# Kernel optimization log

Hardware: AMD Instinct MI355X
Metric: run time of the kernel (lower is better)

Reference implementation:

```python
import jax, jax.numpy as jnp
from jax import lax
import numpy as np

B, H, Wd, CIN, COUT, KH, KW = 64, 64, 64, 128, 256, 3, 3
WSTD, BSTD = 0.3, 0.3
DN = ('NHWC', 'HWIO', 'NHWC')


def setup_inputs() -> dict:
    key = jax.random.key(0)
    k1, k2, k3, k4, k5 = jax.random.split(key, 5)
    X = jax.random.normal(k1, (B, H, Wd, CIN), dtype=jnp.float32)
    W = jax.random.normal(k2, (KH, KW, CIN, COUT), dtype=jnp.float32) * 0.05
    bias = jax.random.normal(k3, (COUT,), dtype=jnp.float32) * 0.05
    # per-sample multiplicative noise: |1 + N(0, std)| as in the original layer
    Werr = jnp.abs(1.0 + WSTD * jax.random.normal(k4, (B, KH, KW, CIN, COUT), dtype=jnp.float32))
    Berr = jnp.abs(1.0 + BSTD * jax.random.normal(k5, (B, COUT), dtype=jnp.float32))
    return {"X": X, "W": W, "bias": bias, "Werr": Werr, "Berr": Berr}


def _conv_single(x, w):
    # x: [H, W, Cin], w: [kh, kw, Cin, Cout] -> [Ho, Wo, Cout], VALID, stride 1
    return lax.conv_general_dilated(x[None], w, window_strides=(1, 1),
                                    padding='VALID', dimension_numbers=DN)[0]


def reference(X, W, bias, Werr, Berr):
    # per-sample noisy filters: memW[b] = W * Werr[b]
    memW = W[None] * Werr                        # [B, kh, kw, Cin, Cout]
    Z = jax.vmap(_conv_single)(X, memW)          # [B, Ho, Wo, Cout]
    membias = bias[None] * Berr                  # [B, Cout]
    return Z + membias[:, None, None, :]
```

## Files before the change

### kernel.cpp

```cpp
#include <hip/hip_runtime.h>
#include <hip/hip_bf16.h>

#define NB   64
#define NH   64
#define NW   64
#define NCI  128
#define NCO  256
#define NHO  62
#define NWO  62
#define MTOT (NHO*NWO)
#define KTOT (9*NCI)

#define BM  128
#define BN  128
#define BK  32

using bf16x8 = __attribute__((ext_vector_type(8))) short;
using f32x4  = __attribute__((ext_vector_type(4))) float;

__device__ __forceinline__ void gload_lds16(const __hip_bfloat16* g,
                                            __hip_bfloat16* l) {
    __builtin_amdgcn_global_load_lds(
        (const __attribute__((address_space(1))) unsigned int*)g,
        (__attribute__((address_space(3))) unsigned int*)l,
        16, 0, 0);
}

__global__ __launch_bounds__(256)
void cvt_x_kernel(const float* __restrict__ X,
                  __hip_bfloat16* __restrict__ Xb, int n8) {
    int i = blockIdx.x * 256 + threadIdx.x;
    if (i >= n8) return;
    const float4* p = (const float4*)X + (size_t)i * 2;
    float4 a = p[0], c = p[1];
    union { __hip_bfloat16 h[8]; float4 v; } u;
    u.h[0] = __float2bfloat16(a.x); u.h[1] = __float2bfloat16(a.y);
    u.h[2] = __float2bfloat16(a.z); u.h[3] = __float2bfloat16(a.w);
    u.h[4] = __float2bfloat16(c.x); u.h[5] = __float2bfloat16(c.y);
    u.h[6] = __float2bfloat16(c.z); u.h[7] = __float2bfloat16(c.w);
    *((float4*)Xb + i) = u.v;
}

#define TK 64
#define TN 64
#define TPAD 65
__global__ __launch_bounds__(256)
void build_wt_kernel(const float* __restrict__ W,
                     const float* __restrict__ Werr,
                     __hip_bfloat16* __restrict__ Wt) {
    __shared__ __hip_bfloat16 tile[TK * TPAD];
    const int t  = threadIdx.x;
    const int b  = blockIdx.z;
    const int k0 = blockIdx.x * TK;
    const int n0 = blockIdx.y * TN;

    const int c4 = (t & 15) * 4;
    const int r  = t >> 4;
    const float* wb = W + n0;
    const float* eb = Werr + (size_t)b * (KTOT * NCO) + n0;
#pragma unroll
    for (int p = 0; p < 4; p++) {
        int k  = k0 + r + p * 16;
        int kl = r + p * 16;
        float4 w = *(const float4*)(wb + (size_t)k * NCO + c4);
        float4 e = *(const float4*)(eb + (size_t)k * NCO + c4);
        tile[kl * TPAD + c4 + 0] = __float2bfloat16(w.x * e.x);
        tile[kl * TPAD + c4 + 1] = __float2bfloat16(w.y * e.y);
        tile[kl * TPAD + c4 + 2] = __float2bfloat16(w.z * e.z);
        tile[kl * TPAD + c4 + 3] = __float2bfloat16(w.w * e.w);
    }
    __syncthreads();
    const int np = t >> 2;
    const int ks = (t & 3) * 16;
    __hip_bfloat16* ob = Wt + ((size_t)b * NCO + n0 + np) * KTOT + k0 + ks;
    union { __hip_bfloat16 h[8]; float4 v; } u;
#pragma unroll
    for (int h2 = 0; h2 < 2; h2++) {
#pragma unroll
        for (int q = 0; q < 8; q++) u.h[q] = tile[(ks + h2 * 8 + q) * TPAD + np];
        *(float4*)(ob + h2 * 8) = u.v;
    }
}

__global__ __launch_bounds__(256)
void gemm_bf16_kernel(const __hip_bfloat16* __restrict__ Xb,
                      const __hip_bfloat16* __restrict__ Wt,
                      const float* __restrict__ bias,
                      const float* __restrict__ Berr,
                      float* __restrict__ out) {
    __shared__ __hip_bfloat16 As[BM * BK];
    __shared__ __hip_bfloat16 Bs[BN * BK];

    const int t    = threadIdx.x;
    const int lane = t & 63;
    const int wave = t >> 6;
    const int b  = blockIdx.y;
    const int nt = blockIdx.x & 1;
    const int mt = blockIdx.x >> 1;
    const int m0 = mt * BM;
    const int n0 = nt * BN;

    const int seg = (lane & 3) * 8;
    const int rl  = lane >> 2;
    const int rA0 = wave * 32 + rl;
    const int rA1 = rA0 + 16;

    int mA0 = m0 + rA0; if (mA0 > MTOT - 1) mA0 = MTOT - 1;
    int mA1 = m0 + rA1; if (mA1 > MTOT - 1) mA1 = MTOT - 1;
    const int oh0 = mA0 / NWO, ow0 = mA0 % NWO;
    const int oh1 = mA1 / NWO, ow1 = mA1 % NWO;
    const __hip_bfloat16* xbase = Xb + (size_t)b * (NH * NW * NCI);
    const __hip_bfloat16* ga0 = xbase + (oh0 * NW + ow0) * NCI + seg;
    const __hip_bfloat16* ga1 = xbase + (oh1 * NW + ow1) * NCI + seg;
    const __hip_bfloat16* wbase = Wt + ((size_t)b * NCO + n0) * KTOT;
    const __hip_bfloat16* gb0 = wbase + rA0 * KTOT + seg;
    const __hip_bfloat16* gb1 = wbase + rA1 * KTOT + seg;

    __hip_bfloat16* lA0 = As + wave * (32 * BK);
    __hip_bfloat16* lA1 = lA0 + 16 * BK;
    __hip_bfloat16* lB0 = Bs + wave * (32 * BK);
    __hip_bfloat16* lB1 = lB0 + 16 * BK;

    const int wm = wave & 1, wn = wave >> 1;
    const int lrow = lane & 15, quad = lane >> 4;
    const int aoff = (wm * 64 + lrow) * BK + quad * 8;
    const int boff = (wn * 64 + lrow) * BK + quad * 8;

    f32x4 acc[4][4];
#pragma unroll
    for (int i = 0; i < 4; i++)
#pragma unroll
        for (int j = 0; j < 4; j++) acc[i][j] = (f32x4){0.f, 0.f, 0.f, 0.f};

    for (int kk = 0; kk < KTOT; kk += BK) {
        const int kh  = kk / (3 * NCI);
        const int kwp = (kk / NCI) % 3;
        const int ci0 = kk % NCI;
        const int ku  = (kh * NW + kwp) * NCI + ci0;

        gload_lds16(ga0 + ku, lA0);
        gload_lds16(ga1 + ku, lA1);
        gload_lds16(gb0 + kk, lB0);
        gload_lds16(gb1 + kk, lB1);
        __syncthreads();

        bf16x8 af[4], bfr[4];
#pragma unroll
        for (int i = 0; i < 4; i++) af[i]  = *(const bf16x8*)&As[aoff + i * 16 * BK];
#pragma unroll
        for (int j = 0; j < 4; j++) bfr[j] = *(const bf16x8*)&Bs[boff + j * 16 * BK];
#pragma unroll
        for (int i = 0; i < 4; i++)
#pragma unroll
            for (int j = 0; j < 4; j++)
                acc[i][j] = __builtin_amdgcn_mfma_f32_16x16x32_bf16(
                    af[i], bfr[j], acc[i][j], 0, 0, 0);
        __syncthreads();
    }

    float bv[4];
#pragma unroll
    for (int j = 0; j < 4; j++) {
        int n = n0 + wn * 64 + j * 16 + lrow;
        bv[j] = bias[n] * Berr[b * NCO + n];
    }
#pragma unroll
    for (int i = 0; i < 4; i++) {
#pragma unroll
        for (int r = 0; r < 4; r++) {
            int m = m0 + wm * 64 + i * 16 + quad * 4 + r;
            if (m < MTOT) {
                float* op = out + ((size_t)b * MTOT + m) * NCO;
#pragma unroll
                for (int j = 0; j < 4; j++) {
                    int n = n0 + wn * 64 + j * 16 + lrow;
                    op[n] = acc[i][j][r] + bv[j];
                }
            }
        }
    }
}

__global__ void naive_conv_kernel(const float* __restrict__ X,
                                  const float* __restrict__ W,
                                  const float* __restrict__ bias,
                                  const float* __restrict__ Werr,
                                  const float* __restrict__ Berr,
                                  float* __restrict__ out) {
    size_t idx = (size_t)blockIdx.x * 256 + threadIdx.x;
    if (idx >= (size_t)NB * MTOT * NCO) return;
    int n = idx % NCO;
    size_t m = idx / NCO;
    int ow = m % NWO; size_t t2 = m / NWO;
    int oh = t2 % NHO; int b = t2 / NHO;
    float acc = bias[n] * Berr[b * NCO + n];
    for (int kh = 0; kh < 3; kh++)
        for (int kw = 0; kw < 3; kw++) {
            const float* xp = X + (((size_t)b * NH + oh + kh) * NW + ow + kw) * NCI;
            const float* wp = W + ((kh * 3 + kw) * NCI) * (size_t)NCO + n;
            const float* ep = Werr + (size_t)b * KTOT * NCO + ((kh * 3 + kw) * NCI) * (size_t)NCO + n;
            for (int ci = 0; ci < NCI; ci++)
                acc += xp[ci] * wp[ci * NCO] * ep[ci * NCO];
        }
    out[idx] = acc;
}

extern "C" void kernel_launch(void* const* d_in, const int* in_sizes, int n_in,
                              void* d_out, int out_size, void* d_ws, size_t ws_size,
                              hipStream_t stream) {
    const float* X    = (const float*)d_in[0];
    const float* W    = (const float*)d_in[1];
    const float* bias = (const float*)d_in[2];
    const float* Werr = (const float*)d_in[3];
    const float* Berr = (const float*)d_in[4];
    float* out = (float*)d_out;

    const size_t xb_bytes = (size_t)NB * NH * NW * NCI * 2;
    const size_t wt_bytes = (size_t)NB * NCO * KTOT * 2;

    if (ws_size < xb_bytes + wt_bytes) {
        size_t total = (size_t)NB * MTOT * NCO;
        naive_conv_kernel<<<(int)((total + 255) / 256), 256, 0, stream>>>(
            X, W, bias, Werr, Berr, out);
        return;
    }

    __hip_bfloat16* Xb = (__hip_bfloat16*)d_ws;
    __hip_bfloat16* Wt = (__hip_bfloat16*)((char*)d_ws + xb_bytes);

    int n8 = NB * NH * NW * NCI / 8;
    cvt_x_kernel<<<n8 / 256, 256, 0, stream>>>(X, Xb, n8);
    build_wt_kernel<<<dim3(KTOT / TK, NCO / TN, NB), 256, 0, stream>>>(W, Werr, Wt);
    gemm_bf16_kernel<<<dim3(2 * ((MTOT + BM - 1) / BM), NB), 256, 0, stream>>>(
        Xb, Wt, bias, Berr, out);
}
```

Before: 590.0 us.

## Rewrite GEMM with 256x256x64 tiles, LDS double buffering, XOR swizzle and block swizzle

```diff
diff --git a/kernel.cpp b/kernel.cpp
--- a/kernel.cpp
+++ b/kernel.cpp
@@ -11,9 +11,11 @@
 #define MTOT (NHO*NWO)
 #define KTOT (9*NCI)
 
-#define BM  128
-#define BN  128
-#define BK  32
+#define BM  256
+#define BN  256
+#define BK  64
+#define NKT (KTOT/BK)
+#define MT  16
 
 using bf16x8 = __attribute__((ext_vector_type(8))) short;
 using f32x4  = __attribute__((ext_vector_type(4))) float;
@@ -25,6 +27,10 @@
         (__attribute__((address_space(3))) unsigned int*)l,
         16, 0, 0);
 }
+
+#define SBAR()   __builtin_amdgcn_s_barrier()
+#define SCHED()  __builtin_amdgcn_sched_barrier(0)
+#define VMCNT(n) asm volatile("s_waitcnt vmcnt(" #n ")" ::: "memory")
 
 __global__ __launch_bounds__(256)
 void cvt_x_kernel(const float* __restrict__ X,
@@ -82,100 +88,125 @@
     }
 }
 
-__global__ __launch_bounds__(256)
+__global__ __launch_bounds__(512, 2)
 void gemm_bf16_kernel(const __hip_bfloat16* __restrict__ Xb,
                       const __hip_bfloat16* __restrict__ Wt,
                       const float* __restrict__ bias,
                       const float* __restrict__ Berr,
                       float* __restrict__ out) {
-    __shared__ __hip_bfloat16 As[BM * BK];
-    __shared__ __hip_bfloat16 Bs[BN * BK];
+    __shared__ __hip_bfloat16 lds[2][2][BM * BK];
 
     const int t    = threadIdx.x;
     const int lane = t & 63;
     const int wave = t >> 6;
-    const int b  = blockIdx.y;
-    const int nt = blockIdx.x & 1;
-    const int mt = blockIdx.x >> 1;
-    const int m0 = mt * BM;
-    const int n0 = nt * BN;
-
-    const int seg = (lane & 3) * 8;
-    const int rl  = lane >> 2;
-    const int rA0 = wave * 32 + rl;
-    const int rA1 = rA0 + 16;
-
-    int mA0 = m0 + rA0; if (mA0 > MTOT - 1) mA0 = MTOT - 1;
-    int mA1 = m0 + rA1; if (mA1 > MTOT - 1) mA1 = MTOT - 1;
-    const int oh0 = mA0 / NWO, ow0 = mA0 % NWO;
-    const int oh1 = mA1 / NWO, ow1 = mA1 % NWO;
+
+    const int bid = blockIdx.x;
+    const int swz = (bid & 7) * ((NB * MT) / 8) + (bid >> 3);
+    const int b   = swz >> 4;
+    const int m0  = (swz & 15) * BM;
+
     const __hip_bfloat16* xbase = Xb + (size_t)b * (NH * NW * NCI);
-    const __hip_bfloat16* ga0 = xbase + (oh0 * NW + ow0) * NCI + seg;
-    const __hip_bfloat16* ga1 = xbase + (oh1 * NW + ow1) * NCI + seg;
-    const __hip_bfloat16* wbase = Wt + ((size_t)b * NCO + n0) * KTOT;
-    const __hip_bfloat16* gb0 = wbase + rA0 * KTOT + seg;
-    const __hip_bfloat16* gb1 = wbase + rA1 * KTOT + seg;
-
-    __hip_bfloat16* lA0 = As + wave * (32 * BK);
-    __hip_bfloat16* lA1 = lA0 + 16 * BK;
-    __hip_bfloat16* lB0 = Bs + wave * (32 * BK);
-    __hip_bfloat16* lB1 = lB0 + 16 * BK;
-
-    const int wm = wave & 1, wn = wave >> 1;
+    const __hip_bfloat16* wbase = Wt + (size_t)b * NCO * KTOT;
+
+    const int srow  = t >> 3;
+    const int gslot = (t & 7) ^ (srow & 7);
+
+    int aoffg[4], boffg[4];
+#pragma unroll
+    for (int l = 0; l < 4; l++) {
+        int row = l * 64 + srow;
+        int m = m0 + row; if (m > MTOT - 1) m = MTOT - 1;
+        int oh = m / NWO, ow = m - oh * NWO;
+        aoffg[l] = (oh * NW + ow) * NCI + gslot * 8;
+        boffg[l] = row * KTOT + gslot * 8;
+    }
+
+    auto STAGE = [&](int buf, int kt) {
+        const int k0 = kt * BK;
+        const int kh = k0 / (3 * NCI);
+        const int rm = k0 - kh * (3 * NCI);
+        const int kw = rm / NCI;
+        const int ci = rm - kw * NCI;
+        const int kuA = (kh * NW + kw) * NCI + ci;
+        __hip_bfloat16* lA = &lds[buf][0][wave * 512];
+        __hip_bfloat16* lB = &lds[buf][1][wave * 512];
+#pragma unroll
+        for (int l = 0; l < 4; l++) {
+            gload_lds16(xbase + aoffg[l] + kuA, lA + l * 4096);
+            gload_lds16(wbase + boffg[l] + k0,  lB + l * 4096);
+        }
+    };
+
     const int lrow = lane & 15, quad = lane >> 4;
-    const int aoff = (wm * 64 + lrow) * BK + quad * 8;
-    const int boff = (wn * 64 + lrow) * BK + quad * 8;
-
-    f32x4 acc[4][4];
-#pragma unroll
-    for (int i = 0; i < 4; i++)
+    const int wm = wave >> 2;
+    const int wn = wave & 3;
+    const int fswz = (lrow & 7) << 3;
+
+    f32x4 acc[8][4];
+#pragma unroll
+    for (int i = 0; i < 8; i++)
 #pragma unroll
         for (int j = 0; j < 4; j++) acc[i][j] = (f32x4){0.f, 0.f, 0.f, 0.f};
 
-    for (int kk = 0; kk < KTOT; kk += BK) {
-        const int kh  = kk / (3 * NCI);
-        const int kwp = (kk / NCI) % 3;
-        const int ci0 = kk % NCI;
-        const int ku  = (kh * NW + kwp) * NCI + ci0;
-
-        gload_lds16(ga0 + ku, lA0);
-        gload_lds16(ga1 + ku, lA1);
-        gload_lds16(gb0 + kk, lB0);
-        gload_lds16(gb1 + kk, lB1);
-        __syncthreads();
-
-        bf16x8 af[4], bfr[4];
-#pragma unroll
-        for (int i = 0; i < 4; i++) af[i]  = *(const bf16x8*)&As[aoff + i * 16 * BK];
-#pragma unroll
-        for (int j = 0; j < 4; j++) bfr[j] = *(const bf16x8*)&Bs[boff + j * 16 * BK];
-#pragma unroll
-        for (int i = 0; i < 4; i++)
+    auto PHASE = [&](int buf, int kk) {
+        const __hip_bfloat16* A  = &lds[buf][0][0];
+        const __hip_bfloat16* Bp = &lds[buf][1][0];
+        const int ks = (kk * 32 + quad * 8) ^ fswz;
+        bf16x8 af[8], bf[4];
+#pragma unroll
+        for (int i = 0; i < 8; i++)
+            af[i] = *(const bf16x8*)&A[(wm * 128 + i * 16 + lrow) * BK + ks];
+#pragma unroll
+        for (int j = 0; j < 4; j++)
+            bf[j] = *(const bf16x8*)&Bp[(wn * 64 + j * 16 + lrow) * BK + ks];
+        __builtin_amdgcn_s_setprio(1);
+#pragma unroll
+        for (int i = 0; i < 8; i++)
 #pragma unroll
             for (int j = 0; j < 4; j++)
                 acc[i][j] = __builtin_amdgcn_mfma_f32_16x16x32_bf16(
-                    af[i], bfr[j], acc[i][j], 0, 0, 0);
-        __syncthreads();
-    }
+                    af[i], bf[j], acc[i][j], 0, 0, 0);
+        __builtin_amdgcn_s_setprio(0);
+    };
+
+    STAGE(0, 0);
+    STAGE(1, 1);
+    VMCNT(8); SCHED();
+    SBAR(); SCHED();
+
+    for (int s = 0; s < NKT / 2 - 1; ++s) {
+        PHASE(0, 0); PHASE(0, 1);
+        SCHED(); SBAR(); SCHED();
+        STAGE(0, 2 * s + 2);
+        VMCNT(8); SCHED();
+        SBAR(); SCHED();
+        PHASE(1, 0); PHASE(1, 1);
+        SCHED(); SBAR(); SCHED();
+        STAGE(1, 2 * s + 3);
+        VMCNT(8); SCHED();
+        SBAR(); SCHED();
+    }
+    PHASE(0, 0); PHASE(0, 1);
+    VMCNT(0); SCHED();
+    SBAR(); SCHED();
+    PHASE(1, 0); PHASE(1, 1);
 
     float bv[4];
 #pragma unroll
     for (int j = 0; j < 4; j++) {
-        int n = n0 + wn * 64 + j * 16 + lrow;
+        int n = wn * 64 + j * 16 + lrow;
         bv[j] = bias[n] * Berr[b * NCO + n];
     }
 #pragma unroll
-    for (int i = 0; i < 4; i++) {
+    for (int i = 0; i < 8; i++) {
 #pragma unroll
         for (int r = 0; r < 4; r++) {
-            int m = m0 + wm * 64 + i * 16 + quad * 4 + r;
+            int m = m0 + wm * 128 + i * 16 + quad * 4 + r;
             if (m < MTOT) {
                 float* op = out + ((size_t)b * MTOT + m) * NCO;
 #pragma unroll
-                for (int j = 0; j < 4; j++) {
-                    int n = n0 + wn * 64 + j * 16 + lrow;
-                    op[n] = acc[i][j][r] + bv[j];
-                }
+                for (int j = 0; j < 4; j++)
+                    op[wn * 64 + j * 16 + lrow] = acc[i][j][r] + bv[j];
             }
         }
     }
@@ -231,6 +262,6 @@
     int n8 = NB * NH * NW * NCI / 8;
     cvt_x_kernel<<<n8 / 256, 256, 0, stream>>>(X, Xb, n8);
     build_wt_kernel<<<dim3(KTOT / TK, NCO / TN, NB), 256, 0, stream>>>(W, Werr, Wt);
-    gemm_bf16_kernel<<<dim3(2 * ((MTOT + BM - 1) / BM), NB), 256, 0, stream>>>(
+    gemm_bf16_kernel<<<dim3(NB * MT), 512, 0, stream>>>(
         Xb, Wt, bias, Berr, out);
 }
```

Result: faster. 533.7 us (-9.5%).
